# Optimization experiments

Measured on AMD Instinct MI355X. Metric: run time of the kernel, lower is better.

Reference implementation:

```python
import jax, jax.numpy as jnp
import numpy as np


def setup_inputs() -> dict:
    key = jax.random.key(0)
    k1, k2, k3 = jax.random.split(key, 3)
    B, C, T = 16, 256, 1024
    inp = jax.random.normal(k1, (B, C, T), dtype=jnp.float32)
    tgt = jax.random.normal(k2, (B, C, T), dtype=jnp.float32)
    mask = jax.random.uniform(k3, (B, T), dtype=jnp.float32)
    return {"inp": inp, "tgt": tgt, "mask": mask}


def reference(inp, tgt, mask):
    # inp, tgt: (B, C, T); mask: (B, T)
    # permute(0,2,1) -> (B, T, C), then mask along T
    x = jnp.transpose(inp, (0, 2, 1)) * mask[:, :, None]  # (B, T, C)
    y = jnp.transpose(tgt, (0, 2, 1)) * mask[:, :, None]  # (B, T, C)
    xy = jnp.einsum('btc,bsc->bts', x, y)  # (B, T, T)
    xx = jnp.einsum('btc,bsc->bts', x, x)  # (B, T, T)
    yy = jnp.einsum('btc,bsc->bts', y, y)  # (B, T, T)
    similarity = 2.0 * xy / (xx + yy)
    loss = jnp.exp(-similarity)
    return jnp.mean(loss)
```

## Files before the change

kernel.cpp:

```cpp
#include <hip/hip_runtime.h>

constexpr int Bc = 16;
constexpr int Cc = 256;
constexpr int Tc = 1024;

typedef __attribute__((ext_vector_type(16))) float f32x16;

__global__ void zero_out_kernel(float* out) { out[0] = 0.0f; }

__device__ inline unsigned f2fp8(float x) {
    unsigned u = __float_as_uint(x);
    unsigned sign = (u >> 24) & 0x80u;
    unsigned au = u & 0x7fffffffu;
    if (au < 0x3c800000u) {
        float m = __uint_as_float(au) * 512.0f;
        unsigned d = (unsigned)(m + 0.5f);
        return (d > 7u) ? (sign | 0x08u) : (sign | d);
    }
    if (au > 0x43e00000u) au = 0x43e00000u;
    au += 0x7ffffu + ((au >> 20) & 1u);
    unsigned e = (au >> 23) - 120u;
    return sign | (e << 3) | ((au >> 20) & 7u);
}

__global__ __launch_bounds__(256) void convert_fp8_kernel(
    const float* __restrict__ inp, const float* __restrict__ tgt,
    unsigned char* __restrict__ PX, unsigned char* __restrict__ PY,
    float* __restrict__ out)
{
    if (blockIdx.x == 0 && threadIdx.x == 0) out[0] = 0.0f;

    __shared__ float tile[32][132];
    const int gid = blockIdx.x;
    const int a  = gid >> 10;
    const int b  = (gid >> 6) & 15;
    const int cs = (gid >> 3) & 7;
    const int tg = gid & 7;
    const int t0 = tg * 128;
    const int tid = threadIdx.x;

    const float* src = a ? tgt : inp;
    unsigned char* dst = a ? PY : PX;

#pragma unroll
    for (int i = 0; i < 4; ++i) {
        const int c  = i * 8 + (tid >> 5);
        const int t4 = (tid & 31) * 4;
        const float4 v = *(const float4*)&src[((size_t)(b * Cc + cs * 32 + c)) * Tc + t0 + t4];
        tile[c][t4 + 0] = v.x; tile[c][t4 + 1] = v.y;
        tile[c][t4 + 2] = v.z; tile[c][t4 + 3] = v.w;
    }
    __syncthreads();

    const int tb  = tid >> 6;
    const int kh  = (tid >> 5) & 1;
    const int row = tid & 31;
    const int t   = tb * 32 + row;
    unsigned un[4];
#pragma unroll
    for (int q = 0; q < 4; ++q) {
        unsigned wv = 0;
#pragma unroll
        for (int jj = 0; jj < 4; ++jj) {
            const int j  = q * 4 + jj;
            const int cp = kh * 8 + (j & 7) + (j >> 3) * 16;
            wv |= f2fp8(tile[cp][t]) << (jj * 8);
        }
        un[q] = wv;
    }
    const size_t off = ((size_t)((b * 8 + cs) * 32 + tg * 4 + tb)) * 1024
                     + kh * 512 + row * 16;
    *(uint4*)(dst + off) = make_uint4(un[0], un[1], un[2], un[3]);
}

#define MF(a, b, c) c = __builtin_amdgcn_mfma_f32_32x32x16_fp8_fp8((a), (b), (c), 0, 0, 0)

__device__ inline float epi_sum(const f32x16& XY, const f32x16& SS) {
    float l = 0.0f;
#pragma unroll
    for (int i = 0; i < 16; ++i) {
        float s = 2.0f * XY[i] * __builtin_amdgcn_rcpf(SS[i]);
        s = fminf(fmaxf(s, -60.0f), 60.0f);
        l += __expf(-s);
    }
    return l;
}

__global__ __launch_bounds__(256, 2) void jvs_fp8_kernel(
    const unsigned char* __restrict__ PX,
    const unsigned char* __restrict__ PY,
    float* __restrict__ out)
{
    const int xcd = blockIdx.x & 7;
    const int idx = blockIdx.x >> 3;
    const int b   = xcd * 2 + (idx >> 6);
    const int r6  = idx & 63;
    const int tb0 = (r6 >> 3) * 4;
    const int sb0 = (r6 & 7) * 4;

    const int tid  = threadIdx.x;
    const int lane = tid & 63;
    const int w    = tid >> 6;
    const int wm   = (w >> 1) * 2;
    const int wn   = (w & 1) * 2;

    const int phase = ((idx >> 3) + (idx & 7) + xcd) & 7;

    const int fo = (lane >> 5) * 512 + (lane & 31) * 16;

    const unsigned char* pax0 = PX + ((size_t)(b * 256 + tb0 + wm + 0)) * 1024 + fo;
    const unsigned char* pax1 = PX + ((size_t)(b * 256 + tb0 + wm + 1)) * 1024 + fo;
    const unsigned char* pay0 = PY + ((size_t)(b * 256 + tb0 + wm + 0)) * 1024 + fo;
    const unsigned char* pay1 = PY + ((size_t)(b * 256 + tb0 + wm + 1)) * 1024 + fo;
    const unsigned char* pbx0 = PX + ((size_t)(b * 256 + sb0 + wn + 0)) * 1024 + fo;
    const unsigned char* pbx1 = PX + ((size_t)(b * 256 + sb0 + wn + 1)) * 1024 + fo;
    const unsigned char* pby0 = PY + ((size_t)(b * 256 + sb0 + wn + 0)) * 1024 + fo;
    const unsigned char* pby1 = PY + ((size_t)(b * 256 + sb0 + wn + 1)) * 1024 + fo;

    f32x16 z;
#pragma unroll
    for (int i = 0; i < 16; ++i) z[i] = 0.0f;
    f32x16 xy00 = z, xy01 = z, xy10 = z, xy11 = z;
    f32x16 ss00 = z, ss01 = z, ss10 = z, ss11 = z;

#pragma unroll
    for (int i = 0; i < 8; ++i) {
        const int cs = (i + phase) & 7;
        const size_t o = (size_t)cs * 32768;
        const long2 ax0 = *(const long2*)(pax0 + o);
        const long2 ax1 = *(const long2*)(pax1 + o);
        const long2 ay0 = *(const long2*)(pay0 + o);
        const long2 ay1 = *(const long2*)(pay1 + o);
        const long2 bx0 = *(const long2*)(pbx0 + o);
        const long2 bx1 = *(const long2*)(pbx1 + o);
        const long2 by0 = *(const long2*)(pby0 + o);
        const long2 by1 = *(const long2*)(pby1 + o);

        MF(ax0.x, bx0.x, ss00); MF(ax0.x, bx1.x, ss01);
        MF(ax1.x, bx0.x, ss10); MF(ax1.x, bx1.x, ss11);
        MF(ay0.x, by0.x, ss00); MF(ay0.x, by1.x, ss01);
        MF(ay1.x, by0.x, ss10); MF(ay1.x, by1.x, ss11);
        MF(ax0.x, by0.x, xy00); MF(ax0.x, by1.x, xy01);
        MF(ax1.x, by0.x, xy10); MF(ax1.x, by1.x, xy11);
        MF(ax0.y, bx0.y, ss00); MF(ax0.y, bx1.y, ss01);
        MF(ax1.y, bx0.y, ss10); MF(ax1.y, bx1.y, ss11);
        MF(ay0.y, by0.y, ss00); MF(ay0.y, by1.y, ss01);
        MF(ay1.y, by0.y, ss10); MF(ay1.y, by1.y, ss11);
        MF(ax0.y, by0.y, xy00); MF(ax0.y, by1.y, xy01);
        MF(ax1.y, by0.y, xy10); MF(ax1.y, by1.y, xy11);
    }

    float local = epi_sum(xy00, ss00) + epi_sum(xy01, ss01)
                + epi_sum(xy10, ss10) + epi_sum(xy11, ss11);

#pragma unroll
    for (int off = 32; off > 0; off >>= 1)
        local += __shfl_down(local, off, 64);

    __shared__ float red[4];
    if (lane == 0) red[w] = local;
    __syncthreads();
    if (tid == 0)
        atomicAdd(out, (red[0] + red[1] + red[2] + red[3])
                       * (1.0f / ((float)Bc * (float)Tc * (float)Tc)));
}

constexpr int TILE = 64;
constexpr int KC   = 16;

__global__ __launch_bounds__(256) void jvs_loss_kernel(
    const float* __restrict__ inp, const float* __restrict__ tgt, float* __restrict__ out)
{
    __shared__ float xs_t[KC][TILE];
    __shared__ float xs_s[KC][TILE];
    __shared__ float ys_t[KC][TILE];
    __shared__ float ys_s[KC][TILE];

    constexpr int NT = Tc / TILE;
    const int blk = blockIdx.x;
    const int b   = blk / (NT * NT);
    const int r   = blk % (NT * NT);
    const int t0  = (r / NT) * TILE;
    const int s0  = (r % NT) * TILE;
    const int tid = threadIdx.x;
    const int tx  = tid & 15;
    const int ty  = tid >> 4;
    const int lrow  = tid >> 4;
    const int lcol4 = tid & 15;
    const float* baseI = inp + (size_t)b * Cc * Tc;
    const float* baseT = tgt + (size_t)b * Cc * Tc;

    float acc_xy[4][4] = {{0.f}}, acc_xx[4][4] = {{0.f}}, acc_yy[4][4] = {{0.f}};
    for (int c0 = 0; c0 < Cc; c0 += KC) {
        __syncthreads();
        const size_t rowOff = (size_t)(c0 + lrow) * Tc;
        *(float4*)&xs_t[lrow][lcol4 * 4] = *(const float4*)(baseI + rowOff + t0 + lcol4 * 4);
        *(float4*)&xs_s[lrow][lcol4 * 4] = *(const float4*)(baseI + rowOff + s0 + lcol4 * 4);
        *(float4*)&ys_t[lrow][lcol4 * 4] = *(const float4*)(baseT + rowOff + t0 + lcol4 * 4);
        *(float4*)&ys_s[lrow][lcol4 * 4] = *(const float4*)(baseT + rowOff + s0 + lcol4 * 4);
        __syncthreads();
#pragma unroll
        for (int kc = 0; kc < KC; ++kc) {
            float xt[4], xsv[4], yt[4], ysv[4];
#pragma unroll
            for (int i = 0; i < 4; ++i) {
                xt[i]  = xs_t[kc][ty * 4 + i];  yt[i]  = ys_t[kc][ty * 4 + i];
                xsv[i] = xs_s[kc][tx * 4 + i];  ysv[i] = ys_s[kc][tx * 4 + i];
            }
#pragma unroll
            for (int i = 0; i < 4; ++i)
#pragma unroll
                for (int j = 0; j < 4; ++j) {
                    acc_xy[i][j] += xt[i] * ysv[j];
                    acc_xx[i][j] += xt[i] * xsv[j];
                    acc_yy[i][j] += yt[i] * ysv[j];
                }
        }
    }
    float local = 0.0f;
#pragma unroll
    for (int i = 0; i < 4; ++i)
#pragma unroll
        for (int j = 0; j < 4; ++j) {
            float sim = 2.0f * acc_xy[i][j] / (acc_xx[i][j] + acc_yy[i][j]);
            sim = fminf(fmaxf(sim, -60.0f), 60.0f);
            local += __expf(-sim);
        }
#pragma unroll
    for (int off = 32; off > 0; off >>= 1) local += __shfl_down(local, off, 64);
    __shared__ float red[4];
    if ((tid & 63) == 0) red[tid >> 6] = local;
    __syncthreads();
    if (tid == 0)
        atomicAdd(out, (red[0] + red[1] + red[2] + red[3])
                       * (1.0f / ((float)Bc * (float)Tc * (float)Tc)));
}

extern "C" void kernel_launch(void* const* d_in, const int* in_sizes, int n_in,
                              void* d_out, int out_size, void* d_ws, size_t ws_size,
                              hipStream_t stream) {
    const float* inp = (const float*)d_in[0];
    const float* tgt = (const float*)d_in[1];
    float* out = (float*)d_out;

    const size_t oneP = (size_t)Bc * Cc * Tc;
    if (ws_size >= 2 * oneP) {
        unsigned char* PX = (unsigned char*)d_ws;
        unsigned char* PY = PX + oneP;
        convert_fp8_kernel<<<2048, 256, 0, stream>>>(inp, tgt, PX, PY, out);
        jvs_fp8_kernel<<<1024, 256, 0, stream>>>(PX, PY, out);
    } else {
        zero_out_kernel<<<1, 1, 0, stream>>>(out);
        jvs_loss_kernel<<<Bc * (Tc / TILE) * (Tc / TILE), 256, 0, stream>>>(inp, tgt, out);
    }
}
```

Before: 102.2 us.

## Exploit symmetry of xx+yy and xy transpose to halve off-diagonal tile work

The denominator xx+yy is symmetric in (t,s), and xy^T(t,s) equals yx(t,s). Each off-diagonal tile pair can therefore be computed once, forward and backward xy together, sharing one denominator, while diagonal tiles keep the full computation. This cuts the MFMA count roughly in half but gives blocks unequal work and adds a small triangular index loop. The fp8 conversion also switches to the hardware cvt_pk_fp8 builtin when the compiler provides it, which may round differently from the software routine.

Result: faster. 99.58 us (-2.5%).

```diff
diff --git a/kernel.cpp b/kernel.cpp
--- a/kernel.cpp
+++ b/kernel.cpp
@@ -23,6 +23,12 @@
     return sign | (e << 3) | ((au >> 20) & 7u);
 }
 
+#if defined(__has_builtin)
+#if __has_builtin(__builtin_amdgcn_cvt_pk_fp8_f32)
+#define HAS_HW_FP8 1
+#endif
+#endif
+
 __global__ __launch_bounds__(256) void convert_fp8_kernel(
     const float* __restrict__ inp, const float* __restrict__ tgt,
     unsigned char* __restrict__ PX, unsigned char* __restrict__ PY,
@@ -59,14 +65,24 @@
     unsigned un[4];
 #pragma unroll
     for (int q = 0; q < 4; ++q) {
-        unsigned wv = 0;
+        float f[4];
 #pragma unroll
         for (int jj = 0; jj < 4; ++jj) {
             const int j  = q * 4 + jj;
             const int cp = kh * 8 + (j & 7) + (j >> 3) * 16;
-            wv |= f2fp8(tile[cp][t]) << (jj * 8);
-        }
+            f[jj] = tile[cp][t];
+        }
+#if defined(HAS_HW_FP8)
+        int v = 0;
+        v = __builtin_amdgcn_cvt_pk_fp8_f32(f[0], f[1], v, false);
+        v = __builtin_amdgcn_cvt_pk_fp8_f32(f[2], f[3], v, true);
+        un[q] = (unsigned)v;
+#else
+        unsigned wv = 0;
+#pragma unroll
+        for (int jj = 0; jj < 4; ++jj) wv |= f2fp8(f[jj]) << (jj * 8);
         un[q] = wv;
+#endif
     }
     const size_t off = ((size_t)((b * 8 + cs) * 32 + tg * 4 + tb)) * 1024
                      + kh * 512 + row * 16;
@@ -82,6 +98,20 @@
         float s = 2.0f * XY[i] * __builtin_amdgcn_rcpf(SS[i]);
         s = fminf(fmaxf(s, -60.0f), 60.0f);
         l += __expf(-s);
+    }
+    return l;
+}
+
+__device__ inline float epi_pair(const f32x16& XF, const f32x16& XB, const f32x16& SS) {
+    float l = 0.0f;
+#pragma unroll
+    for (int i = 0; i < 16; ++i) {
+        const float r = 2.0f * __builtin_amdgcn_rcpf(SS[i]);
+        float s1 = XF[i] * r;
+        float s2 = XB[i] * r;
+        s1 = fminf(fmaxf(s1, -60.0f), 60.0f);
+        s2 = fminf(fmaxf(s2, -60.0f), 60.0f);
+        l += __expf(-s1) + __expf(-s2);
     }
     return l;
 }
@@ -91,67 +121,115 @@
     const unsigned char* __restrict__ PY,
     float* __restrict__ out)
 {
-    const int xcd = blockIdx.x & 7;
-    const int idx = blockIdx.x >> 3;
+    const int bid = blockIdx.x;
+    const int xcd = bid & 7;
+    const int idx = bid >> 3;
     const int b   = xcd * 2 + (idx >> 6);
-    const int r6  = idx & 63;
-    const int tb0 = (r6 >> 3) * 4;
-    const int sb0 = (r6 & 7) * 4;
+    const int u   = idx & 63;
 
     const int tid  = threadIdx.x;
     const int lane = tid & 63;
-    const int w    = tid >> 6;
-    const int wm   = (w >> 1) * 2;
-    const int wn   = (w & 1) * 2;
+    const int w    = __builtin_amdgcn_readfirstlane(tid >> 6);
 
     const int phase = ((idx >> 3) + (idx & 7) + xcd) & 7;
 
     const int fo = (lane >> 5) * 512 + (lane & 31) * 16;
-
-    const unsigned char* pax0 = PX + ((size_t)(b * 256 + tb0 + wm + 0)) * 1024 + fo;
-    const unsigned char* pax1 = PX + ((size_t)(b * 256 + tb0 + wm + 1)) * 1024 + fo;
-    const unsigned char* pay0 = PY + ((size_t)(b * 256 + tb0 + wm + 0)) * 1024 + fo;
-    const unsigned char* pay1 = PY + ((size_t)(b * 256 + tb0 + wm + 1)) * 1024 + fo;
-    const unsigned char* pbx0 = PX + ((size_t)(b * 256 + sb0 + wn + 0)) * 1024 + fo;
-    const unsigned char* pbx1 = PX + ((size_t)(b * 256 + sb0 + wn + 1)) * 1024 + fo;
-    const unsigned char* pby0 = PY + ((size_t)(b * 256 + sb0 + wn + 0)) * 1024 + fo;
-    const unsigned char* pby1 = PY + ((size_t)(b * 256 + sb0 + wn + 1)) * 1024 + fo;
+    const size_t bbase = (size_t)b * 262144;
 
     f32x16 z;
 #pragma unroll
     for (int i = 0; i < 16; ++i) z[i] = 0.0f;
-    f32x16 xy00 = z, xy01 = z, xy10 = z, xy11 = z;
-    f32x16 ss00 = z, ss01 = z, ss10 = z, ss11 = z;
-
-#pragma unroll
-    for (int i = 0; i < 8; ++i) {
-        const int cs = (i + phase) & 7;
-        const size_t o = (size_t)cs * 32768;
-        const long2 ax0 = *(const long2*)(pax0 + o);
-        const long2 ax1 = *(const long2*)(pax1 + o);
-        const long2 ay0 = *(const long2*)(pay0 + o);
-        const long2 ay1 = *(const long2*)(pay1 + o);
-        const long2 bx0 = *(const long2*)(pbx0 + o);
-        const long2 bx1 = *(const long2*)(pbx1 + o);
-        const long2 by0 = *(const long2*)(pby0 + o);
-        const long2 by1 = *(const long2*)(pby1 + o);
-
-        MF(ax0.x, bx0.x, ss00); MF(ax0.x, bx1.x, ss01);
-        MF(ax1.x, bx0.x, ss10); MF(ax1.x, bx1.x, ss11);
-        MF(ay0.x, by0.x, ss00); MF(ay0.x, by1.x, ss01);
-        MF(ay1.x, by0.x, ss10); MF(ay1.x, by1.x, ss11);
-        MF(ax0.x, by0.x, xy00); MF(ax0.x, by1.x, xy01);
-        MF(ax1.x, by0.x, xy10); MF(ax1.x, by1.x, xy11);
-        MF(ax0.y, bx0.y, ss00); MF(ax0.y, bx1.y, ss01);
-        MF(ax1.y, bx0.y, ss10); MF(ax1.y, bx1.y, ss11);
-        MF(ay0.y, by0.y, ss00); MF(ay0.y, by1.y, ss01);
-        MF(ay1.y, by0.y, ss10); MF(ay1.y, by1.y, ss11);
-        MF(ax0.y, by0.y, xy00); MF(ax0.y, by1.y, xy01);
-        MF(ax1.y, by0.y, xy10); MF(ax1.y, by1.y, xy11);
-    }
-
-    float local = epi_sum(xy00, ss00) + epi_sum(xy01, ss01)
-                + epi_sum(xy10, ss10) + epi_sum(xy11, ss11);
+
+    float local = 0.0f;
+
+    if (u < 56) {
+        const int q = u >> 1;
+        const int h = u & 1;
+        int gt = 0, rem = q;
+        while (rem >= 7 - gt) { rem -= 7 - gt; ++gt; }
+        const int gs = gt + 1 + rem;
+
+        const int tb = gt * 4 + (w >> 1) * 2;
+        const int sb = gs * 4 + h * 2 + (w & 1);
+
+        const unsigned char* pax0 = PX + bbase + (size_t)(tb + 0) * 1024 + fo;
+        const unsigned char* pax1 = PX + bbase + (size_t)(tb + 1) * 1024 + fo;
+        const unsigned char* pay0 = PY + bbase + (size_t)(tb + 0) * 1024 + fo;
+        const unsigned char* pay1 = PY + bbase + (size_t)(tb + 1) * 1024 + fo;
+        const unsigned char* pbx  = PX + bbase + (size_t)sb * 1024 + fo;
+        const unsigned char* pby  = PY + bbase + (size_t)sb * 1024 + fo;
+
+        f32x16 ss0 = z, ss1 = z;
+        f32x16 xf0 = z, xf1 = z;
+        f32x16 xb0 = z, xb1 = z;
+
+#pragma unroll
+        for (int i = 0; i < 8; ++i) {
+            const int cs = (i + phase) & 7;
+            const size_t o = (size_t)cs * 32768;
+            const long2 ax0 = *(const long2*)(pax0 + o);
+            const long2 ax1 = *(const long2*)(pax1 + o);
+            const long2 ay0 = *(const long2*)(pay0 + o);
+            const long2 ay1 = *(const long2*)(pay1 + o);
+            const long2 bx  = *(const long2*)(pbx  + o);
+            const long2 by  = *(const long2*)(pby  + o);
+
+            MF(ax0.x, bx.x, ss0); MF(ax1.x, bx.x, ss1);
+            MF(ax0.x, by.x, xf0); MF(ax1.x, by.x, xf1);
+            MF(ay0.x, by.x, ss0); MF(ay1.x, by.x, ss1);
+            MF(ay0.x, bx.x, xb0); MF(ay1.x, bx.x, xb1);
+            MF(ax0.y, bx.y, ss0); MF(ax1.y, bx.y, ss1);
+            MF(ax0.y, by.y, xf0); MF(ax1.y, by.y, xf1);
+            MF(ay0.y, by.y, ss0); MF(ay1.y, by.y, ss1);
+            MF(ay0.y, bx.y, xb0); MF(ay1.y, bx.y, xb1);
+        }
+        local = epi_pair(xf0, xb0, ss0) + epi_pair(xf1, xb1, ss1);
+    } else {
+        const int g  = u - 56;
+        const int tb = g * 4 + (w >> 1) * 2;
+        const int sb = g * 4 + (w & 1) * 2;
+
+        const unsigned char* pax0 = PX + bbase + (size_t)(tb + 0) * 1024 + fo;
+        const unsigned char* pax1 = PX + bbase + (size_t)(tb + 1) * 1024 + fo;
+        const unsigned char* pay0 = PY + bbase + (size_t)(tb + 0) * 1024 + fo;
+        const unsigned char* pay1 = PY + bbase + (size_t)(tb + 1) * 1024 + fo;
+        const unsigned char* pbx0 = PX + bbase + (size_t)(sb + 0) * 1024 + fo;
+        const unsigned char* pbx1 = PX + bbase + (size_t)(sb + 1) * 1024 + fo;
+        const unsigned char* pby0 = PY + bbase + (size_t)(sb + 0) * 1024 + fo;
+        const unsigned char* pby1 = PY + bbase + (size_t)(sb + 1) * 1024 + fo;
+
+        f32x16 xy00 = z, xy01 = z, xy10 = z, xy11 = z;
+        f32x16 ss00 = z, ss01 = z, ss10 = z, ss11 = z;
+
+#pragma unroll
+        for (int i = 0; i < 8; ++i) {
+            const int cs = (i + phase) & 7;
+            const size_t o = (size_t)cs * 32768;
+            const long2 ax0 = *(const long2*)(pax0 + o);
+            const long2 ax1 = *(const long2*)(pax1 + o);
+            const long2 ay0 = *(const long2*)(pay0 + o);
+            const long2 ay1 = *(const long2*)(pay1 + o);
+            const long2 bx0 = *(const long2*)(pbx0 + o);
+            const long2 bx1 = *(const long2*)(pbx1 + o);
+            const long2 by0 = *(const long2*)(pby0 + o);
+            const long2 by1 = *(const long2*)(pby1 + o);
+
+            MF(ax0.x, bx0.x, ss00); MF(ax0.x, bx1.x, ss01);
+            MF(ax1.x, bx0.x, ss10); MF(ax1.x, bx1.x, ss11);
+            MF(ay0.x, by0.x, ss00); MF(ay0.x, by1.x, ss01);
+            MF(ay1.x, by0.x, ss10); MF(ay1.x, by1.x, ss11);
+            MF(ax0.x, by0.x, xy00); MF(ax0.x, by1.x, xy01);
+            MF(ax1.x, by0.x, xy10); MF(ax1.x, by1.x, xy11);
+            MF(ax0.y, bx0.y, ss00); MF(ax0.y, bx1.y, ss01);
+            MF(ax1.y, bx0.y, ss10); MF(ax1.y, bx1.y, ss11);
+            MF(ay0.y, by0.y, ss00); MF(ay0.y, by1.y, ss01);
+            MF(ay1.y, by0.y, ss10); MF(ay1.y, by1.y, ss11);
+            MF(ax0.y, by0.y, xy00); MF(ax0.y, by1.y, xy01);
+            MF(ax1.y, by0.y, xy10); MF(ax1.y, by1.y, xy11);
+        }
+        local = epi_sum(xy00, ss00) + epi_sum(xy01, ss01)
+              + epi_sum(xy10, ss10) + epi_sum(xy11, ss11);
+    }
 
 #pragma unroll
     for (int off = 32; off > 0; off >>= 1)
```
